# Performance work log

Hardware: AMD Instinct MI355X
Metric: run time of the kernel (lower is better)

Reference implementation:

```python
import jax, jax.numpy as jnp
import numpy as np

P = 16          # patch size
ER = 2          # expand_ratio = per-head dim in Hgru2

def _shift2d(x, sh, sw):
    # zero-fill shift of (B,C,H,W) image by (sh, sw); matches torch F.pad((l,r,t,b)) with a negative crop
    H, W = x.shape[2], x.shape[3]
    ah, aw = abs(sh), abs(sw)
    xp = jnp.pad(x, ((0, 0), (0, 0), (ah, ah), (aw, aw)))
    return xp[:, :, ah - sh:ah - sh + H, aw - sw:aw - sw + W]

def _layernorm(x, g, b, eps=1e-5):
    m = jnp.mean(x, axis=-1, keepdims=True)
    v = jnp.var(x, axis=-1, keepdims=True)
    return (x - m) * jax.lax.rsqrt(v + eps) * g + b

def _rmsnorm(x, eps=1e-6):
    # FastSimpleRMSNorm: weightless RMS normalization
    return x * jax.lax.rsqrt(jnp.mean(x * x, axis=-1, keepdims=True) + eps)

def _hgru2(x, lb_vec, wi, wo):
    # x: (N, T, D). NOTE: the torch module unpacks x.shape as (n, b, d), so the
    # gated linear recurrence scans over axis 0 exactly as the original does.
    N, T, D = x.shape
    H = D // ER
    feat = x @ wi                                    # (N, T, 3D)
    V, Q, Fg = jnp.split(feat, 3, axis=-1)
    V = jax.nn.gelu(V, approximate=False).reshape(N, T, H, ER)
    Q = jax.nn.gelu(Q, approximate=False).reshape(N, T, H, ER)
    Fg = jax.nn.sigmoid(Fg).reshape(N, T, H, ER)
    lb = lb_vec.reshape(H, ER)
    lam = lb + (1.0 - lb) * Fg                       # decay lambda_t in (lb, 1)
    K = 1.0 - lam
    def step(S, inp):
        q, k, v, l = inp                             # each (T, H, ER)
        # S[t,h,i,j] = lam[i] * S + k[i] * v[j]  (GLA recurrence, 2x2 state/head)
        S = l[..., None] * S + k[..., None] * v[..., None, :]
        o = jnp.einsum('thi,thij->thj', q, S)
        return S, o
    S0 = jnp.zeros((T, H, ER, ER), dtype=x.dtype)
    _, o = jax.lax.scan(step, S0, (Q, K, V, lam))    # o: (N, T, H, ER)
    return o.reshape(N, T, D) @ wo

def reference(img, spt_ln_g, spt_ln_b, spt_w, spt_b, pos_emb, cls_token, lower_bounds,
              in_proj_w, out_proj_w, ff_w1, ff_b1, ff_w2, ff_b2,
              head_ln_g, head_ln_b, head_w, head_b):
    B, C, Hh, Ww = img.shape
    # SPT: concat original + 4 shifted copies on channel axis -> (B, 5C, H, W)
    xs = jnp.concatenate([img,
                          _shift2d(img, 0, 1), _shift2d(img, 0, -1),
                          _shift2d(img, 1, 0), _shift2d(img, -1, 0)], axis=1)
    c5 = 5 * C
    h, w = Hh // P, Ww // P
    # 'b c (h p1) (w p2) -> b (h w) (p1 p2 c)'
    patches = xs.reshape(B, c5, h, P, w, P).transpose(0, 2, 4, 3, 5, 1).reshape(B, h * w, P * P * c5)
    tokens = _layernorm(patches, spt_ln_g, spt_ln_b) @ spt_w + spt_b   # (B, NP, D)
    n = tokens.shape[1]
    cls = jnp.broadcast_to(cls_token, (B, 1, tokens.shape[2]))
    x = jnp.concatenate([cls, tokens], axis=1) + pos_emb[:, :n + 1]
    # layer-wise monotone lower bounds for the decay gate
    lb = jax.nn.softmax(lower_bounds, axis=0)
    lb = jnp.cumsum(lb, axis=0)
    lb = lb - lb[0]
    depth = lower_bounds.shape[0]
    for i in range(depth):
        x = _hgru2(_rmsnorm(x), lb[i], in_proj_w[i], out_proj_w[i]) + x
        hmid = jax.nn.gelu(_rmsnorm(x) @ ff_w1[i] + ff_b1[i], approximate=False)
        x = hmid @ ff_w2[i] + ff_b2[i] + x
    x = _rmsnorm(x)
    x = x[:, 0]                                      # cls pooling
    return _layernorm(x, head_ln_g, head_ln_b) @ head_w + head_b

def setup_inputs():
    key = jax.random.key(0)
    ks = jax.random.split(key, 10)
    B, C, IMG, D, DEPTH, MLP, NC = 16, 3, 256, 768, 8, 3072, 1000
    NP = (IMG // P) ** 2
    PD = P * P * 5 * C
    s = 0.02
    return {
        'img': jax.random.normal(ks[0], (B, C, IMG, IMG), jnp.float32),
        'spt_ln_g': jnp.ones((PD,), jnp.float32),
        'spt_ln_b': jnp.zeros((PD,), jnp.float32),
        'spt_w': jax.random.normal(ks[1], (PD, D), jnp.float32) * s,
        'spt_b': jnp.zeros((D,), jnp.float32),
        'pos_emb': jax.random.normal(ks[2], (1, NP + 1, D), jnp.float32),
        'cls_token': jax.random.normal(ks[3], (1, 1, D), jnp.float32),
        'lower_bounds': jnp.ones((DEPTH, D), jnp.float32),
        'in_proj_w': jax.random.normal(ks[4], (DEPTH, D, 3 * D), jnp.float32) * s,
        'out_proj_w': jax.random.normal(ks[5], (DEPTH, D, D), jnp.float32) * s,
        'ff_w1': jax.random.normal(ks[6], (DEPTH, D, MLP), jnp.float32) * s,
        'ff_b1': jnp.zeros((DEPTH, MLP), jnp.float32),
        'ff_w2': jax.random.normal(ks[7], (DEPTH, MLP, D), jnp.float32) * s,
        'ff_b2': jnp.zeros((DEPTH, D), jnp.float32),
        'head_ln_g': jnp.ones((D,), jnp.float32),
        'head_ln_b': jnp.zeros((D,), jnp.float32),
        'head_w': jax.random.normal(ks[8], (D, NC), jnp.float32) * s,
        'head_b': jnp.zeros((NC,), jnp.float32),
    }
```

## Files before the change

kernel.cpp:

```cpp
#include <hip/hip_runtime.h>
#include <hip/hip_bf16.h>

typedef __bf16 bf16x8 __attribute__((ext_vector_type(8)));
typedef float floatx4 __attribute__((ext_vector_type(4)));

#define DEV __device__ __forceinline__

DEV float gelu_f(float x) {
    return 0.5f * x * (1.0f + erff(x * 0.70710678118654752f));
}

DEV void block_reduce2(float& a, float& b, float* s) {
    #pragma unroll
    for (int o = 32; o > 0; o >>= 1) {
        a += __shfl_down(a, o, 64);
        b += __shfl_down(b, o, 64);
    }
    __syncthreads();
    int wv = threadIdx.x >> 6;
    if ((threadIdx.x & 63) == 0) { s[wv * 2] = a; s[wv * 2 + 1] = b; }
    __syncthreads();
    int nw = blockDim.x >> 6;
    float ra = 0.f, rb = 0.f;
    for (int i = 0; i < nw; ++i) { ra += s[i * 2]; rb += s[i * 2 + 1]; }
    a = ra; b = rb;
}

__global__ __launch_bounds__(256) void compute_lb(const float* __restrict__ lbin, float* __restrict__ lbout) {
    int d = blockIdx.x * 256 + threadIdx.x;
    if (d >= 768) return;
    float v[8];
    float mx = -1e30f;
    #pragma unroll
    for (int i = 0; i < 8; ++i) { v[i] = lbin[i * 768 + d]; mx = fmaxf(mx, v[i]); }
    float s = 0.f;
    #pragma unroll
    for (int i = 0; i < 8; ++i) { v[i] = expf(v[i] - mx); s += v[i]; }
    float inv = 1.f / s;
    float first = v[0] * inv;
    float cum = 0.f;
    #pragma unroll
    for (int i = 0; i < 8; ++i) { cum += v[i] * inv; lbout[i * 768 + d] = cum - first; }
}

__global__ __launch_bounds__(256) void init_tokens(const float* __restrict__ cls, const float* __restrict__ pos,
                                                   const float* __restrict__ bias, float* __restrict__ x) {
    int i = blockIdx.x * 256 + threadIdx.x;
    if (i >= 16 * 257 * 768) return;
    int d = i % 768;
    int row = i / 768;
    int t = row % 257;
    float v;
    if (t == 0) v = cls[d] + pos[d];
    else        v = bias[d] + pos[(size_t)t * 768 + d];
    x[(size_t)row * 768 + d] = v;
}

__global__ __launch_bounds__(256) void patch_ln(const float* __restrict__ img, const float* __restrict__ g,
                                                const float* __restrict__ bt, __hip_bfloat16* __restrict__ out) {
    int pm = blockIdx.x;
    int b = pm >> 8, pp = pm & 255;
    int ph = pp >> 4, pw = pp & 15;
    __shared__ float pv[3840];
    __shared__ float sbuf[8];
    float s = 0.f, ss = 0.f;
    #pragma unroll
    for (int i = 0; i < 15; ++i) {
        int f = threadIdx.x + i * 256;
        int pi = f / 15, cc = f % 15;
        int ip = pi >> 4, jp = pi & 15;
        int g5 = cc / 3, ch = cc % 3;
        int sh = (g5 == 3) - (g5 == 4);
        int sw = (g5 == 1) - (g5 == 2);
        int y = ph * 16 + ip - sh;
        int x = pw * 16 + jp - sw;
        float val = 0.f;
        if ((unsigned)y < 256u && (unsigned)x < 256u)
            val = img[(((size_t)b * 3 + ch) * 256 + y) * 256 + x];
        pv[f] = val; s += val; ss += val * val;
    }
    block_reduce2(s, ss, sbuf);
    float mean = s * (1.f / 3840.f);
    float var  = ss * (1.f / 3840.f) - mean * mean;
    float inv  = rsqrtf(var + 1e-5f);
    #pragma unroll
    for (int i = 0; i < 15; ++i) {
        int f = threadIdx.x + i * 256;
        out[(size_t)pm * 3840 + f] = __float2bfloat16((pv[f] - mean) * inv * g[f] + bt[f]);
    }
}

__global__ __launch_bounds__(256) void transpose_cast(const float* __restrict__ W, __hip_bfloat16* __restrict__ Wt,
                                                      int K, int N) {
    __shared__ float tile[32][33];
    int k0 = blockIdx.x * 32, n0 = blockIdx.y * 32;
    int tx = threadIdx.x & 31, ty = threadIdx.x >> 5;
    #pragma unroll
    for (int i = 0; i < 4; ++i) {
        int k = ty + i * 8;
        tile[k][tx] = W[(size_t)(k0 + k) * N + n0 + tx];
    }
    __syncthreads();
    #pragma unroll
    for (int i = 0; i < 4; ++i) {
        int n = ty + i * 8;
        Wt[(size_t)(n0 + n) * K + k0 + tx] = __float2bfloat16(tile[tx][n]);
    }
}

__global__ __launch_bounds__(256) void rmsnorm_kernel(const float* __restrict__ x, __hip_bfloat16* __restrict__ out) {
    int row = blockIdx.x;
    const float* xr = x + (size_t)row * 768;
    __shared__ float sbuf[8];
    float v[3];
    float ss = 0.f, d0 = 0.f;
    #pragma unroll
    for (int i = 0; i < 3; ++i) { v[i] = xr[threadIdx.x + i * 256]; ss += v[i] * v[i]; }
    block_reduce2(ss, d0, sbuf);
    float scale = rsqrtf(ss * (1.f / 768.f) + 1e-6f);
    #pragma unroll
    for (int i = 0; i < 3; ++i)
        out[(size_t)row * 768 + threadIdx.x + i * 256] = __float2bfloat16(v[i] * scale);
}

__global__ __launch_bounds__(256) void hgru_scan(const float* __restrict__ feat, __hip_bfloat16* __restrict__ o) {
    int idx = blockIdx.x * 256 + threadIdx.x;
    if (idx >= 257 * 384) return;
    int t = idx / 384, h = idx % 384;
    float2 V[16], Q[16], L[16];
    #pragma unroll
    for (int n = 0; n < 16; ++n) {
        size_t base = ((size_t)n * 257 + t) * 2304 + h * 2;
        V[n] = *(const float2*)(feat + base);
        Q[n] = *(const float2*)(feat + base + 768);
        L[n] = *(const float2*)(feat + base + 1536);
    }
    float S00 = 0.f, S01 = 0.f, S10 = 0.f, S11 = 0.f;
    #pragma unroll
    for (int n = 0; n < 16; ++n) {
        float l0 = L[n].x, l1 = L[n].y;
        float k0 = 1.f - l0, k1 = 1.f - l1;
        S00 = l0 * S00 + k0 * V[n].x; S01 = l0 * S01 + k0 * V[n].y;
        S10 = l1 * S10 + k1 * V[n].x; S11 = l1 * S11 + k1 * V[n].y;
        float o0 = Q[n].x * S00 + Q[n].y * S10;
        float o1 = Q[n].x * S01 + Q[n].y * S11;
        __hip_bfloat162 ov;
        ov.x = __float2bfloat16(o0);
        ov.y = __float2bfloat16(o1);
        *(__hip_bfloat162*)(o + ((size_t)n * 257 + t) * 768 + h * 2) = ov;
    }
}

__global__ __launch_bounds__(256) void head_kernel(const float* __restrict__ x, const float* __restrict__ g,
                                                   const float* __restrict__ be, const float* __restrict__ hw,
                                                   const float* __restrict__ hb, float* __restrict__ out) {
    int b = blockIdx.x;
    const float* xr = x + (size_t)b * 257 * 768;
    __shared__ float z[768];
    __shared__ float sbuf[8];
    float v[3];
    float ss = 0.f, d0 = 0.f;
    #pragma unroll
    for (int i = 0; i < 3; ++i) { v[i] = xr[threadIdx.x + i * 256]; ss += v[i] * v[i]; }
    block_reduce2(ss, d0, sbuf);
    float rs = rsqrtf(ss * (1.f / 768.f) + 1e-6f);
    float s = 0.f, s2 = 0.f;
    #pragma unroll
    for (int i = 0; i < 3; ++i) { float y = v[i] * rs; s += y; s2 += y * y; }
    block_reduce2(s, s2, sbuf);
    float mean = s * (1.f / 768.f);
    float var  = s2 * (1.f / 768.f) - mean * mean;
    float inv  = rsqrtf(var + 1e-5f);
    #pragma unroll
    for (int i = 0; i < 3; ++i) {
        int d = threadIdx.x + i * 256;
        z[d] = (v[i] * rs - mean) * inv * g[d] + be[d];
    }
    __syncthreads();
    int j = blockIdx.y * 256 + threadIdx.x;
    if (j < 1000) {
        float acc = hb[j];
        for (int d = 0; d < 768; ++d) acc += z[d] * hw[d * 1000 + j];
        out[b * 1000 + j] = acc;
    }
}

template<int EPI, int BN>
__global__ __launch_bounds__(256) void gemm_bt(
        const __hip_bfloat16* __restrict__ A, const __hip_bfloat16* __restrict__ Bt,
        int N, int Ktot, int Mvalid,
        float* __restrict__ outf, __hip_bfloat16* __restrict__ outb,
        const float* __restrict__ bias, const float* __restrict__ aux) {
    constexpr int WNF = BN / 32;
    __shared__ alignas(16) __hip_bfloat16 Als[3][128 * 32];
    __shared__ alignas(16) __hip_bfloat16 Bls[3][BN * 32];
    const int tid  = threadIdx.x;
    const int lane = tid & 63;
    const int wv   = tid >> 6;

    const int gx = gridDim.x;
    const int nwg = gx * gridDim.y;
    const int orig = blockIdx.x + gx * blockIdx.y;
    const int q = nwg >> 3, r = nwg & 7;
    const int xcd = orig & 7, off = orig >> 3;
    const int wg = (xcd < r ? xcd * (q + 1) : r * (q + 1) + (xcd - r) * q) + off;
    const int n0 = (wg % gx) * BN;
    const int m0 = (wg / gx) * 128;

    const int wm = wv & 1, wn = wv >> 1;
    const int fr = lane & 15;
    const int fq = lane >> 4;
    const int srow = lane >> 2;
    const int scol = (lane & 3) * 8;

    floatx4 acc[4][WNF];
    #pragma unroll
    for (int mi = 0; mi < 4; ++mi)
        #pragma unroll
        for (int ni = 0; ni < WNF; ++ni)
            acc[mi][ni] = (floatx4){0.f, 0.f, 0.f, 0.f};

    auto stage = [&](int kt, int buf) {
        #pragma unroll
        for (int j = 0; j < 2; ++j) {
            int cc = wv * 2 + j;
            const __hip_bfloat16* ga = A + (size_t)(m0 + cc * 16 + srow) * Ktot + kt + scol;
            __builtin_amdgcn_global_load_lds((const __attribute__((address_space(1))) void*)ga,
                                             (__attribute__((address_space(3))) void*)(&Als[buf][cc * 512]), 16, 0, 0);
        }
        #pragma unroll
        for (int j = 0; j < BN / 64; ++j) {
            int cc = wv * (BN / 64) + j;
            const __hip_bfloat16* gb = Bt + (size_t)(n0 + cc * 16 + srow) * Ktot + kt + scol;
            __builtin_amdgcn_global_load_lds((const __attribute__((address_space(1))) void*)gb,
                                             (__attribute__((address_space(3))) void*)(&Bls[buf][cc * 512]), 16, 0, 0);
        }
    };

    const int nk = Ktot / 32;
    stage(0, 0);
    stage(32, 1);

    int cur = 0, sb = 2;
    for (int i = 0; i < nk; ++i) {
        if (i + 1 < nk) {
            if constexpr (BN == 128) asm volatile("s_waitcnt vmcnt(4)" ::: "memory");
            else                     asm volatile("s_waitcnt vmcnt(3)" ::: "memory");
        } else {
            asm volatile("s_waitcnt vmcnt(0)" ::: "memory");
        }
        __builtin_amdgcn_s_barrier();
        __builtin_amdgcn_sched_barrier(0);

        bf16x8 af[4], bfv[WNF];
        #pragma unroll
        for (int mi = 0; mi < 4; ++mi)
            af[mi] = *(const bf16x8*)((const void*)&Als[cur][(wm * 64 + mi * 16 + fr) * 32 + fq * 8]);
        #pragma unroll
        for (int ni = 0; ni < WNF; ++ni)
            bfv[ni] = *(const bf16x8*)((const void*)&Bls[cur][(wn * (BN / 2) + ni * 16 + fr) * 32 + fq * 8]);

        if (i + 2 < nk) stage((i + 2) * 32, sb);

        #pragma unroll
        for (int mi = 0; mi < 4; ++mi)
            #pragma unroll
            for (int ni = 0; ni < WNF; ++ni)
                acc[mi][ni] = __builtin_amdgcn_mfma_f32_16x16x32_bf16(af[mi], bfv[ni], acc[mi][ni], 0, 0, 0);

        cur = (cur == 2) ? 0 : cur + 1;
        sb  = (sb  == 2) ? 0 : sb  + 1;
    }

    const int cr0 = wm * 64 + fq * 4;
    const int cc0 = wn * (BN / 2) + fr;
    #pragma unroll
    for (int mi = 0; mi < 4; ++mi) {
        #pragma unroll
        for (int rr = 0; rr < 4; ++rr) {
            int gm = m0 + cr0 + mi * 16 + rr;
            if (gm >= Mvalid) continue;
            #pragma unroll
            for (int ni = 0; ni < WNF; ++ni) {
                int gn = n0 + cc0 + ni * 16;
                float v = acc[mi][ni][rr];
                if (EPI == 1) {
                    float res;
                    if (gn < 1536) {
                        res = gelu_f(v);
                    } else {
                        float l = aux[gn - 1536];
                        res = l + (1.f - l) / (1.f + expf(-v));
                    }
                    outf[(size_t)gm * N + gn] = res;
                } else if (EPI == 3) {
                    outb[(size_t)gm * N + gn] = __float2bfloat16(gelu_f(v + bias[gn]));
                } else if (EPI == 6) {
                    float add = v + (bias ? bias[gn] : 0.f);
                    outf[(size_t)gm * N + gn] += add;
                } else if (EPI == 7) {
                    size_t orow = (size_t)(gm >> 8) * 257 + 1 + (gm & 255);
                    outf[orow * 768 + gn] += v;
                }
            }
        }
    }
}

extern "C" void kernel_launch(void* const* d_in, const int* in_sizes, int n_in,
                              void* d_out, int out_size, void* d_ws, size_t ws_size,
                              hipStream_t stream) {
    const float* img        = (const float*)d_in[0];
    const float* spt_ln_g   = (const float*)d_in[1];
    const float* spt_ln_b   = (const float*)d_in[2];
    const float* spt_w      = (const float*)d_in[3];
    const float* spt_b      = (const float*)d_in[4];
    const float* pos_emb    = (const float*)d_in[5];
    const float* cls_token  = (const float*)d_in[6];
    const float* lower_bnds = (const float*)d_in[7];
    const float* in_proj_w  = (const float*)d_in[8];
    const float* out_proj_w = (const float*)d_in[9];
    const float* ff_w1      = (const float*)d_in[10];
    const float* ff_b1      = (const float*)d_in[11];
    const float* ff_w2      = (const float*)d_in[12];
    const float* ff_b2      = (const float*)d_in[13];
    const float* head_ln_g  = (const float*)d_in[14];
    const float* head_ln_b  = (const float*)d_in[15];
    const float* head_w     = (const float*)d_in[16];
    const float* head_b     = (const float*)d_in[17];
    float* out = (float*)d_out;

    char* wp = (char*)d_ws;
    auto alloc = [&](size_t bytes) -> void* {
        void* p = (void*)wp;
        wp += (bytes + 255) & ~(size_t)255;
        return p;
    };
    float*          lbbuf   = (float*)         alloc(8 * 768 * 4);
    __hip_bfloat16* patches = (__hip_bfloat16*)alloc((size_t)4096 * 3840 * 2);
    __hip_bfloat16* spt_wt  = (__hip_bfloat16*)alloc((size_t)768 * 3840 * 2);
    float*          xbuf    = (float*)         alloc((size_t)4112 * 768 * 4);
    __hip_bfloat16* normbuf = (__hip_bfloat16*)alloc((size_t)4224 * 768 * 2);
    float*          featbuf = (float*)         alloc((size_t)4112 * 2304 * 4);
    __hip_bfloat16* obuf    = (__hip_bfloat16*)alloc((size_t)4224 * 768 * 2);
    __hip_bfloat16* midbuf  = (__hip_bfloat16*)alloc((size_t)4224 * 3072 * 2);
    __hip_bfloat16* w_in_t  = (__hip_bfloat16*)alloc((size_t)2304 * 768 * 2);
    __hip_bfloat16* w_out_t = (__hip_bfloat16*)alloc((size_t)768 * 768 * 2);
    __hip_bfloat16* w1_t    = (__hip_bfloat16*)alloc((size_t)3072 * 768 * 2);
    __hip_bfloat16* w2_t    = (__hip_bfloat16*)alloc((size_t)768 * 3072 * 2);
    (void)in_sizes; (void)n_in; (void)out_size; (void)ws_size;

    compute_lb<<<3, 256, 0, stream>>>(lower_bnds, lbbuf);
    init_tokens<<<(16 * 257 * 768 + 255) / 256, 256, 0, stream>>>(cls_token, pos_emb, spt_b, xbuf);
    patch_ln<<<4096, 256, 0, stream>>>(img, spt_ln_g, spt_ln_b, patches);
    transpose_cast<<<dim3(3840 / 32, 768 / 32), 256, 0, stream>>>(spt_w, spt_wt, 3840, 768);
    gemm_bt<7, 64><<<dim3(12, 32), 256, 0, stream>>>(patches, spt_wt, 768, 3840, 4096,
                                                     xbuf, nullptr, nullptr, nullptr);

    for (int i = 0; i < 8; ++i) {
        rmsnorm_kernel<<<4112, 256, 0, stream>>>(xbuf, normbuf);
        transpose_cast<<<dim3(24, 72), 256, 0, stream>>>(in_proj_w + (size_t)i * 768 * 2304, w_in_t, 768, 2304);
        gemm_bt<1, 128><<<dim3(18, 33), 256, 0, stream>>>(normbuf, w_in_t, 2304, 768, 4112,
                                                          featbuf, nullptr, nullptr, lbbuf + i * 768);
        hgru_scan<<<386, 256, 0, stream>>>(featbuf, obuf);
        transpose_cast<<<dim3(24, 24), 256, 0, stream>>>(out_proj_w + (size_t)i * 768 * 768, w_out_t, 768, 768);
        gemm_bt<6, 64><<<dim3(12, 33), 256, 0, stream>>>(obuf, w_out_t, 768, 768, 4112,
                                                         xbuf, nullptr, nullptr, nullptr);
        rmsnorm_kernel<<<4112, 256, 0, stream>>>(xbuf, normbuf);
        transpose_cast<<<dim3(24, 96), 256, 0, stream>>>(ff_w1 + (size_t)i * 768 * 3072, w1_t, 768, 3072);
        gemm_bt<3, 128><<<dim3(24, 33), 256, 0, stream>>>(normbuf, w1_t, 3072, 768, 4112,
                                                          nullptr, midbuf, ff_b1 + i * 3072, nullptr);
        transpose_cast<<<dim3(96, 24), 256, 0, stream>>>(ff_w2 + (size_t)i * 3072 * 768, w2_t, 3072, 768);
        gemm_bt<6, 64><<<dim3(12, 33), 256, 0, stream>>>(midbuf, w2_t, 768, 3072, 4112,
                                                         xbuf, nullptr, ff_b2 + i * 768, nullptr);
    }

    head_kernel<<<dim3(16, 4), 256, 0, stream>>>(xbuf, head_ln_g, head_ln_b, head_w, head_b, out);
}
```

Baseline: 1.883 ms.

## Use K=64 GEMM tiles with XOR-swizzled LDS and vectorized weight transpose

Replaces the GEMM with a variant that stages 64-wide K slices into LDS using an XOR swizzle, so each barrier covers twice as many MFMAs and LDS bank conflicts on fragment reads go down. All GEMMs now use a 128x64 output tile, which changes grid shapes for the in-proj and FF1 GEMMs (previously 128x128). The weight transpose-cast kernel now uses 64x64 tiles with float4 loads and 4-wide bf16 stores. LDS use per block rises to 72 KB, which may limit occupancy, and narrower tiles give less reuse on the wide GEMMs.

```diff
diff --git a/kernel.cpp b/kernel.cpp
--- a/kernel.cpp
+++ b/kernel.cpp
@@ -90,21 +90,35 @@
     }
 }
 
-__global__ __launch_bounds__(256) void transpose_cast(const float* __restrict__ W, __hip_bfloat16* __restrict__ Wt,
-                                                      int K, int N) {
-    __shared__ float tile[32][33];
-    int k0 = blockIdx.x * 32, n0 = blockIdx.y * 32;
-    int tx = threadIdx.x & 31, ty = threadIdx.x >> 5;
+__global__ __launch_bounds__(256) void transpose_cast64(const float* __restrict__ W, __hip_bfloat16* __restrict__ Wt,
+                                                        int K, int N) {
+    __shared__ float tile[64][65];
+    int k0 = blockIdx.x * 64, n0 = blockIdx.y * 64;
+    int tx = threadIdx.x & 15;
+    int ty = threadIdx.x >> 4;
     #pragma unroll
     for (int i = 0; i < 4; ++i) {
-        int k = ty + i * 8;
-        tile[k][tx] = W[(size_t)(k0 + k) * N + n0 + tx];
+        int k = ty + i * 16;
+        float4 v = *(const float4*)&W[(size_t)(k0 + k) * N + n0 + tx * 4];
+        tile[k][tx * 4 + 0] = v.x;
+        tile[k][tx * 4 + 1] = v.y;
+        tile[k][tx * 4 + 2] = v.z;
+        tile[k][tx * 4 + 3] = v.w;
     }
     __syncthreads();
     #pragma unroll
     for (int i = 0; i < 4; ++i) {
-        int n = ty + i * 8;
-        Wt[(size_t)(n0 + n) * K + k0 + tx] = __float2bfloat16(tile[tx][n]);
+        int n = ty + i * 16;
+        __hip_bfloat16 b0 = __float2bfloat16(tile[tx * 4 + 0][n]);
+        __hip_bfloat16 b1 = __float2bfloat16(tile[tx * 4 + 1][n]);
+        __hip_bfloat16 b2 = __float2bfloat16(tile[tx * 4 + 2][n]);
+        __hip_bfloat16 b3 = __float2bfloat16(tile[tx * 4 + 3][n]);
+        ushort4 o;
+        o.x = *reinterpret_cast<unsigned short*>(&b0);
+        o.y = *reinterpret_cast<unsigned short*>(&b1);
+        o.z = *reinterpret_cast<unsigned short*>(&b2);
+        o.w = *reinterpret_cast<unsigned short*>(&b3);
+        *(ushort4*)&Wt[(size_t)(n0 + n) * K + k0 + tx * 4] = o;
     }
 }
 
@@ -185,15 +199,14 @@
     }
 }
 
-template<int EPI, int BN>
-__global__ __launch_bounds__(256) void gemm_bt(
+template<int EPI>
+__global__ __launch_bounds__(256) void gemm64(
         const __hip_bfloat16* __restrict__ A, const __hip_bfloat16* __restrict__ Bt,
         int N, int Ktot, int Mvalid,
         float* __restrict__ outf, __hip_bfloat16* __restrict__ outb,
         const float* __restrict__ bias, const float* __restrict__ aux) {
-    constexpr int WNF = BN / 32;
-    __shared__ alignas(16) __hip_bfloat16 Als[3][128 * 32];
-    __shared__ alignas(16) __hip_bfloat16 Bls[3][BN * 32];
+    __shared__ alignas(16) __hip_bfloat16 Als[3][128 * 64];
+    __shared__ alignas(16) __hip_bfloat16 Bls[3][64 * 64];
     const int tid  = threadIdx.x;
     const int lane = tid & 63;
     const int wv   = tid >> 6;
@@ -204,76 +217,86 @@
     const int q = nwg >> 3, r = nwg & 7;
     const int xcd = orig & 7, off = orig >> 3;
     const int wg = (xcd < r ? xcd * (q + 1) : r * (q + 1) + (xcd - r) * q) + off;
-    const int n0 = (wg % gx) * BN;
+    const int n0 = (wg % gx) * 64;
     const int m0 = (wg / gx) * 128;
 
     const int wm = wv & 1, wn = wv >> 1;
     const int fr = lane & 15;
     const int fq = lane >> 4;
-    const int srow = lane >> 2;
-    const int scol = (lane & 3) * 8;
-
-    floatx4 acc[4][WNF];
+    const int srow8 = lane >> 3;
+    const int slot8 = lane & 7;
+    const int sswz  = (slot8 ^ srow8) * 8;
+
+    floatx4 acc[4][2];
     #pragma unroll
     for (int mi = 0; mi < 4; ++mi)
         #pragma unroll
-        for (int ni = 0; ni < WNF; ++ni)
+        for (int ni = 0; ni < 2; ++ni)
             acc[mi][ni] = (floatx4){0.f, 0.f, 0.f, 0.f};
 
+    const __hip_bfloat16* pA0 = A  + (size_t)(m0 + wv * 8      + srow8) * Ktot + sswz;
+    const __hip_bfloat16* pA1 = A  + (size_t)(m0 + wv * 8 + 32 + srow8) * Ktot + sswz;
+    const __hip_bfloat16* pA2 = A  + (size_t)(m0 + wv * 8 + 64 + srow8) * Ktot + sswz;
+    const __hip_bfloat16* pA3 = A  + (size_t)(m0 + wv * 8 + 96 + srow8) * Ktot + sswz;
+    const __hip_bfloat16* pB0 = Bt + (size_t)(n0 + wv * 8      + srow8) * Ktot + sswz;
+    const __hip_bfloat16* pB1 = Bt + (size_t)(n0 + wv * 8 + 32 + srow8) * Ktot + sswz;
+
     auto stage = [&](int kt, int buf) {
-        #pragma unroll
-        for (int j = 0; j < 2; ++j) {
-            int cc = wv * 2 + j;
-            const __hip_bfloat16* ga = A + (size_t)(m0 + cc * 16 + srow) * Ktot + kt + scol;
-            __builtin_amdgcn_global_load_lds((const __attribute__((address_space(1))) void*)ga,
-                                             (__attribute__((address_space(3))) void*)(&Als[buf][cc * 512]), 16, 0, 0);
-        }
-        #pragma unroll
-        for (int j = 0; j < BN / 64; ++j) {
-            int cc = wv * (BN / 64) + j;
-            const __hip_bfloat16* gb = Bt + (size_t)(n0 + cc * 16 + srow) * Ktot + kt + scol;
-            __builtin_amdgcn_global_load_lds((const __attribute__((address_space(1))) void*)gb,
-                                             (__attribute__((address_space(3))) void*)(&Bls[buf][cc * 512]), 16, 0, 0);
-        }
+        __hip_bfloat16* la = &Als[buf][(wv * 8) * 64 + lane * 8];
+        __hip_bfloat16* lb = &Bls[buf][(wv * 8) * 64 + lane * 8];
+        __builtin_amdgcn_global_load_lds((const __attribute__((address_space(1))) void*)(pA0 + kt),
+                                         (__attribute__((address_space(3))) void*)(la),            16, 0, 0);
+        __builtin_amdgcn_global_load_lds((const __attribute__((address_space(1))) void*)(pA1 + kt),
+                                         (__attribute__((address_space(3))) void*)(la + 32 * 64),  16, 0, 0);
+        __builtin_amdgcn_global_load_lds((const __attribute__((address_space(1))) void*)(pA2 + kt),
+                                         (__attribute__((address_space(3))) void*)(la + 64 * 64),  16, 0, 0);
+        __builtin_amdgcn_global_load_lds((const __attribute__((address_space(1))) void*)(pA3 + kt),
+                                         (__attribute__((address_space(3))) void*)(la + 96 * 64),  16, 0, 0);
+        __builtin_amdgcn_global_load_lds((const __attribute__((address_space(1))) void*)(pB0 + kt),
+                                         (__attribute__((address_space(3))) void*)(lb),            16, 0, 0);
+        __builtin_amdgcn_global_load_lds((const __attribute__((address_space(1))) void*)(pB1 + kt),
+                                         (__attribute__((address_space(3))) void*)(lb + 32 * 64),  16, 0, 0);
     };
 
-    const int nk = Ktot / 32;
+    const int nk = Ktot / 64;
     stage(0, 0);
-    stage(32, 1);
-
-    int cur = 0, sb = 2;
+    stage(64, 1);
+
+    const int rx = fr & 7;
+    int cur = 0;
     for (int i = 0; i < nk; ++i) {
-        if (i + 1 < nk) {
-            if constexpr (BN == 128) asm volatile("s_waitcnt vmcnt(4)" ::: "memory");
-            else                     asm volatile("s_waitcnt vmcnt(3)" ::: "memory");
-        } else {
-            asm volatile("s_waitcnt vmcnt(0)" ::: "memory");
-        }
+        if (i + 1 < nk) asm volatile("s_waitcnt vmcnt(6)" ::: "memory");
+        else            asm volatile("s_waitcnt vmcnt(0)" ::: "memory");
         __builtin_amdgcn_s_barrier();
         __builtin_amdgcn_sched_barrier(0);
 
-        bf16x8 af[4], bfv[WNF];
+        bf16x8 af[2][4], bfv[2][2];
         #pragma unroll
-        for (int mi = 0; mi < 4; ++mi)
-            af[mi] = *(const bf16x8*)((const void*)&Als[cur][(wm * 64 + mi * 16 + fr) * 32 + fq * 8]);
+        for (int s = 0; s < 2; ++s) {
+            int slot = ((s * 4 + fq) ^ rx) * 8;
+            #pragma unroll
+            for (int mi = 0; mi < 4; ++mi)
+                af[s][mi] = *(const bf16x8*)((const void*)&Als[cur][(wm * 64 + mi * 16 + fr) * 64 + slot]);
+            #pragma unroll
+            for (int ni = 0; ni < 2; ++ni)
+                bfv[s][ni] = *(const bf16x8*)((const void*)&Bls[cur][(wn * 32 + ni * 16 + fr) * 64 + slot]);
+        }
+
+        if (i + 2 < nk) stage((i + 2) * 64, cur == 0 ? 2 : cur - 1);
+
         #pragma unroll
-        for (int ni = 0; ni < WNF; ++ni)
-            bfv[ni] = *(const bf16x8*)((const void*)&Bls[cur][(wn * (BN / 2) + ni * 16 + fr) * 32 + fq * 8]);
-
-        if (i + 2 < nk) stage((i + 2) * 32, sb);
-
-        #pragma unroll
-        for (int mi = 0; mi < 4; ++mi)
+        for (int s = 0; s < 2; ++s)
             #pragma unroll
-            for (int ni = 0; ni < WNF; ++ni)
-                acc[mi][ni] = __builtin_amdgcn_mfma_f32_16x16x32_bf16(af[mi], bfv[ni], acc[mi][ni], 0, 0, 0);
+            for (int mi = 0; mi < 4; ++mi)
+                #pragma unroll
+                for (int ni = 0; ni < 2; ++ni)
+                    acc[mi][ni] = __builtin_amdgcn_mfma_f32_16x16x32_bf16(af[s][mi], bfv[s][ni], acc[mi][ni], 0, 0, 0);
 
         cur = (cur == 2) ? 0 : cur + 1;
-        sb  = (sb  == 2) ? 0 : sb  + 1;
     }
 
     const int cr0 = wm * 64 + fq * 4;
-    const int cc0 = wn * (BN / 2) + fr;
+    const int cc0 = wn * 32 + fr;
     #pragma unroll
     for (int mi = 0; mi < 4; ++mi) {
         #pragma unroll
@@ -281,7 +304,7 @@
             int gm = m0 + cr0 + mi * 16 + rr;
             if (gm >= Mvalid) continue;
             #pragma unroll
-            for (int ni = 0; ni < WNF; ++ni) {
+            for (int ni = 0; ni < 2; ++ni) {
                 int gn = n0 + cc0 + ni * 16;
                 float v = acc[mi][ni][rr];
                 if (EPI == 1) {
@@ -353,26 +376,26 @@
     compute_lb<<<3, 256, 0, stream>>>(lower_bnds, lbbuf);
     init_tokens<<<(16 * 257 * 768 + 255) / 256, 256, 0, stream>>>(cls_token, pos_emb, spt_b, xbuf);
     patch_ln<<<4096, 256, 0, stream>>>(img, spt_ln_g, spt_ln_b, patches);
-    transpose_cast<<<dim3(3840 / 32, 768 / 32), 256, 0, stream>>>(spt_w, spt_wt, 3840, 768);
-    gemm_bt<7, 64><<<dim3(12, 32), 256, 0, stream>>>(patches, spt_wt, 768, 3840, 4096,
-                                                     xbuf, nullptr, nullptr, nullptr);
+    transpose_cast64<<<dim3(3840 / 64, 768 / 64), 256, 0, stream>>>(spt_w, spt_wt, 3840, 768);
+    gemm64<7><<<dim3(12, 32), 256, 0, stream>>>(patches, spt_wt, 768, 3840, 4096,
+                                                xbuf, nullptr, nullptr, nullptr);
 
     for (int i = 0; i < 8; ++i) {
         rmsnorm_kernel<<<4112, 256, 0, stream>>>(xbuf, normbuf);
-        transpose_cast<<<dim3(24, 72), 256, 0, stream>>>(in_proj_w + (size_t)i * 768 * 2304, w_in_t, 768, 2304);
-        gemm_bt<1, 128><<<dim3(18, 33), 256, 0, stream>>>(normbuf, w_in_t, 2304, 768, 4112,
-                                                          featbuf, nullptr, nullptr, lbbuf + i * 768);
+        transpose_cast64<<<dim3(12, 36), 256, 0, stream>>>(in_proj_w + (size_t)i * 768 * 2304, w_in_t, 768, 2304);
+        gemm64<1><<<dim3(36, 33), 256, 0, stream>>>(normbuf, w_in_t, 2304, 768, 4112,
+                                                    featbuf, nullptr, nullptr, lbbuf + i * 768);
         hgru_scan<<<386, 256, 0, stream>>>(featbuf, obuf);
-        transpose_cast<<<dim3(24, 24), 256, 0, stream>>>(out_proj_w + (size_t)i * 768 * 768, w_out_t, 768, 768);
-        gemm_bt<6, 64><<<dim3(12, 33), 256, 0, stream>>>(obuf, w_out_t, 768, 768, 4112,
-                                                         xbuf, nullptr, nullptr, nullptr);
+        transpose_cast64<<<dim3(12, 12), 256, 0, stream>>>(out_proj_w + (size_t)i * 768 * 768, w_out_t, 768, 768);
+        gemm64<6><<<dim3(12, 33), 256, 0, stream>>>(obuf, w_out_t, 768, 768, 4112,
+                                                    xbuf, nullptr, nullptr, nullptr);
         rmsnorm_kernel<<<4112, 256, 0, stream>>>(xbuf, normbuf);
-        transpose_cast<<<dim3(24, 96), 256, 0, stream>>>(ff_w1 + (size_t)i * 768 * 3072, w1_t, 768, 3072);
-        gemm_bt<3, 128><<<dim3(24, 33), 256, 0, stream>>>(normbuf, w1_t, 3072, 768, 4112,
-                                                          nullptr, midbuf, ff_b1 + i * 3072, nullptr);
-        transpose_cast<<<dim3(96, 24), 256, 0, stream>>>(ff_w2 + (size_t)i * 3072 * 768, w2_t, 3072, 768);
-        gemm_bt<6, 64><<<dim3(12, 33), 256, 0, stream>>>(midbuf, w2_t, 768, 3072, 4112,
-                                                         xbuf, nullptr, ff_b2 + i * 768, nullptr);
+        transpose_cast64<<<dim3(12, 48), 256, 0, stream>>>(ff_w1 + (size_t)i * 768 * 3072, w1_t, 768, 3072);
+        gemm64<3><<<dim3(48, 33), 256, 0, stream>>>(normbuf, w1_t, 3072, 768, 4112,
+                                                    nullptr, midbuf, ff_b1 + i * 3072, nullptr);
+        transpose_cast64<<<dim3(48, 12), 256, 0, stream>>>(ff_w2 + (size_t)i * 3072 * 768, w2_t, 3072, 768);
+        gemm64<6><<<dim3(12, 33), 256, 0, stream>>>(midbuf, w2_t, 768, 3072, 4112,
+                                                    xbuf, nullptr, ff_b2 + i * 768, nullptr);
     }
 
     head_kernel<<<dim3(16, 4), 256, 0, stream>>>(xbuf, head_ln_g, head_ln_b, head_w, head_b, out);
```

Result: faster. 1.811 ms (-3.8%).
